# Kernel optimization log

Hardware: AMD Instinct MI355X
Metric: run time of the kernel (lower is better)

Reference implementation:

```python
import jax, jax.numpy as jnp
import numpy as np

HEADS = 8
BLOCK = 32

def setup_inputs() -> dict:
    key = jax.random.key(0)
    ks = jax.random.split(key, 4)
    b, n, d, f = 4, 4096, 1024, 128
    x = jax.random.normal(ks[0], (b, n, d), dtype=jnp.float32)
    w_qkv = jax.random.normal(ks[1], (3 * d, d), dtype=jnp.float32) * (d ** -0.5)
    w_out = jax.random.normal(ks[2], (d, d), dtype=jnp.float32) * (d ** -0.5)
    b_out = jnp.zeros((d,), dtype=jnp.float32)
    proj = jax.random.normal(ks[3], (HEADS, d // HEADS, f), dtype=jnp.float32) * ((d // HEADS) ** -0.5)
    return {"x": x, "w_qkv": w_qkv, "w_out": w_out, "b_out": b_out, "proj": proj}

def reference(x, w_qkv, w_out, b_out, proj):
    b, n, d = x.shape
    h = HEADS
    hd = d // h
    nb = n // BLOCK
    # QKV projection (torch Linear: x @ W.T)
    qkv = x @ w_qkv.T  # (b, n, 3d)
    q, k, v = jnp.split(qkv, 3, axis=-1)
    def to_blocks(t):
        # (b, n, d) -> (b, h, nb, BLOCK, hd)
        return t.reshape(b, n, h, hd).transpose(0, 2, 1, 3).reshape(b, h, nb, BLOCK, hd)
    q, k, v = to_blocks(q), to_blocks(k), to_blocks(v)
    # per-head feature map: elu(x @ proj) + 1
    qp = jax.nn.elu(jnp.einsum('bhcsd,hdf->bhcsf', q, proj)) + 1.0
    kp = jax.nn.elu(jnp.einsum('bhcsd,hdf->bhcsf', k, proj)) + 1.0
    # per-block kv state and normalizer
    kv = jnp.einsum('bhcsf,bhcsd->bhcfd', kp, v)          # (b,h,nb,f,hd)
    num = jnp.einsum('bhcsf,bhcfd->bhcsd', qp, kv)        # (b,h,nb,BLOCK,hd)
    ksum = kp.sum(axis=3)                                 # (b,h,nb,f)
    z = 1.0 / (jnp.einsum('bhcsf,bhcf->bhcs', qp, ksum) + 1e-8)
    out = num * z[..., None]
    # merge blocks and heads: (b,h,nb,BLOCK,hd) -> (b,n,d)
    out = out.reshape(b, h, n, hd).transpose(0, 2, 1, 3).reshape(b, n, d)
    # output projection (dropout inert in eval)
    return out @ w_out.T + b_out
```

## Files before the change

kernel.cpp:

```cpp
#include <hip/hip_runtime.h>
#include <hip/hip_bf16.h>
#include <stdint.h>
#include <stddef.h>

typedef __bf16 bf16_t;
typedef __bf16 bf16x8 __attribute__((ext_vector_type(8)));
typedef __bf16 bf16x4 __attribute__((ext_vector_type(4)));
typedef float  f32x4  __attribute__((ext_vector_type(4)));

static __device__ __forceinline__ f32x4 mfma16x16x32(bf16x8 a, bf16x8 b, f32x4 c) {
  return __builtin_amdgcn_mfma_f32_16x16x32_bf16(a, b, c, 0, 0, 0);
}

static __device__ __forceinline__ void gld_lds16(const void* g, void* l) {
  __builtin_amdgcn_global_load_lds(
      (const __attribute__((address_space(1))) unsigned int*)g,
      (__attribute__((address_space(3))) unsigned int*)l, 16, 0, 0);
}

#define BARW()   __builtin_amdgcn_s_barrier()
#define SCHED0() __builtin_amdgcn_sched_barrier(0)
#define LGKM0()  asm volatile("s_waitcnt lgkmcnt(0)" ::: "memory")
#define LGKMN(n) asm volatile("s_waitcnt lgkmcnt(" #n ")" ::: "memory")
#define VMCNT(n) asm volatile("s_waitcnt vmcnt(" #n ")" ::: "memory")
#define PRIO(p)  __builtin_amdgcn_s_setprio(p)

__global__ __launch_bounds__(256) void prep(const float* __restrict__ wqkv,
                                            const float* __restrict__ proj,
                                            const float* __restrict__ wout,
                                            const float* __restrict__ x,
                                            bf16_t* __restrict__ B1t2,
                                            bf16_t* __restrict__ Wv,
                                            bf16_t* __restrict__ W3t,
                                            bf16_t* __restrict__ xbf) {
  const int b = blockIdx.x;
  const int tid = threadIdx.x;
  if (b >= 1536) {
    for (int i = (b - 1536) * 256 + tid; i < 4194304; i += 262144) {
      float4 v = *(const float4*)(x + (size_t)i * 4);
      bf16x4 o;
      o[0] = (bf16_t)v.x; o[1] = (bf16_t)v.y; o[2] = (bf16_t)v.z; o[3] = (bf16_t)v.w;
      *(bf16x4*)(xbf + (size_t)i * 4) = o;
    }
    return;
  }
  if (b >= 1024) {
    const float* src = (b < 1280) ? wout : (wqkv + (size_t)2048 * 1024);
    bf16_t* dst = (b < 1280) ? W3t : Wv;
    size_t off = ((size_t)((b - 1024) & 255) * 4096) + tid * 16;
#pragma unroll
    for (int it = 0; it < 4; ++it) {
      float4 v = *(const float4*)(src + off + it * 4);
      bf16x4 o;
      o[0] = (bf16_t)v.x; o[1] = (bf16_t)v.y; o[2] = (bf16_t)v.z; o[3] = (bf16_t)v.w;
      *(bf16x4*)(dst + off + it * 4) = o;
    }
    return;
  }
  const int combo = b >> 6;
  const int kt    = (b >> 2) & 15;
  const int fq    = b & 3;
  const int qk    = combo >> 3;
  const int h     = combo & 7;
  const int klocal = tid & 63;
  const int fg     = tid >> 6;
  const int k      = kt * 64 + klocal;

  const float* wbase = wqkv + ((size_t)(qk * 1024 + h * 128)) * 1024 + k;
  const float* pbase = proj + (size_t)h * 16384 + fq * 32 + fg * 8;

  float acc[8];
#pragma unroll
  for (int i = 0; i < 8; ++i) acc[i] = 0.f;

  for (int c = 0; c < 128; ++c) {
    float a = wbase[(size_t)c * 1024];
    const float4* p = (const float4*)(pbase + (size_t)c * 128);
    float4 p0 = p[0], p1 = p[1];
    acc[0] += a * p0.x; acc[1] += a * p0.y; acc[2] += a * p0.z; acc[3] += a * p0.w;
    acc[4] += a * p1.x; acc[5] += a * p1.y; acc[6] += a * p1.z; acc[7] += a * p1.w;
  }
  bf16_t* obase = B1t2 + ((size_t)(h * 256 + qk * 128 + fq * 32 + fg * 8)) * 1024 + k;
#pragma unroll
  for (int i = 0; i < 8; ++i) obase[(size_t)i * 1024] = (bf16_t)acc[i];
}

#define GEMM_MAINLOOP_DECLS()                                                  \
  const int tid  = threadIdx.x;                                                \
  const int lane = tid & 63;                                                   \
  const int wid  = tid >> 6;                                                   \
  const int wm   = wid >> 2;                                                   \
  const int wn   = wid & 3;                                                    \
  const int lr   = lane & 15;                                                  \
  const int g0   = lane >> 4;                                                  \
  int srow[2], sgl[2];                                                         \
  _Pragma("unroll")                                                            \
  for (int l = 0; l < 2; ++l) {                                                \
    int idx = l * 512 + tid;                                                   \
    srow[l] = idx >> 3;                                                        \
    sgl[l]  = (idx & 7) ^ (srow[l] & 7);                                       \
  }

#define STAGE_T(arr, base, half, kt, K_)                                       \
  {                                                                            \
    const bf16_t* s_ = (base) + (size_t)((half) * 128) * (K_) + (kt) * 64;     \
    bf16_t* d_ = &(arr)[half][0];                                              \
    _Pragma("unroll")                                                          \
    for (int l_ = 0; l_ < 2; ++l_)                                             \
      gld_lds16(s_ + (size_t)srow[l_] * (K_) + sgl[l_] * 8,                    \
                d_ + (l_ * 512 + tid) * 8);                                    \
  }

#define RD_A(buf, qm)                                                          \
  _Pragma("unroll")                                                            \
  for (int t_ = 0; t_ < 4; ++t_) {                                             \
    int r_ = (qm) * 64 + t_ * 16 + lr;                                         \
    _Pragma("unroll")                                                          \
    for (int kh_ = 0; kh_ < 2; ++kh_) {                                        \
      int gl_ = (g0 + kh_ * 4) ^ (r_ & 7);                                     \
      a[t_][kh_] = *(const bf16x8*)(&sA[buf][wm][r_ * 64 + gl_ * 8]);          \
    }                                                                          \
  }
#define RD_B(buf, qn, breg)                                                    \
  _Pragma("unroll")                                                            \
  for (int u_ = 0; u_ < 2; ++u_) {                                             \
    int r_ = (wn & 1) * 64 + (qn) * 32 + u_ * 16 + lr;                         \
    _Pragma("unroll")                                                          \
    for (int kh_ = 0; kh_ < 2; ++kh_) {                                        \
      int gl_ = (g0 + kh_ * 4) ^ (r_ & 7);                                     \
      breg[u_][kh_] = *(const bf16x8*)(&sB[buf][wn >> 1][r_ * 64 + gl_ * 8]);  \
    }                                                                          \
  }
#define MMA(qm, qn, breg)                                                      \
  _Pragma("unroll")                                                            \
  for (int mi_ = 0; mi_ < 4; ++mi_)                                            \
    _Pragma("unroll")                                                          \
    for (int nj_ = 0; nj_ < 2; ++nj_)                                          \
      _Pragma("unroll")                                                        \
      for (int kh_ = 0; kh_ < 2; ++kh_)                                        \
        acc[(qm) * 4 + mi_][(qn) * 2 + nj_] =                                  \
            mfma16x16x32(a[mi_][kh_], breg[nj_][kh_],                          \
                         acc[(qm) * 4 + mi_][(qn) * 2 + nj_]);

#define GEMM_MAINLOOP_BODY(Abase, Bbase, K_, NT_)                              \
  f32x4 acc[8][4] = {};                                                        \
  bf16x8 a[4][2], b0[2][2], b1[2][2];                                          \
  STAGE_T(sA[0], Abase, 0, 0, K_); STAGE_T(sA[0], Abase, 1, 0, K_);            \
  STAGE_T(sB[0], Bbase, 0, 0, K_); STAGE_T(sB[0], Bbase, 1, 0, K_);            \
  STAGE_T(sA[1], Abase, 0, 1, K_); STAGE_T(sA[1], Abase, 1, 1, K_);            \
  STAGE_T(sB[1], Bbase, 0, 1, K_); STAGE_T(sB[1], Bbase, 1, 1, K_);            \
  VMCNT(8);                                                                    \
  BARW();                                                                      \
  _Pragma("unroll 2")                                                          \
  for (int j = 0; j < (NT_); ++j) {                                            \
    const int cur = j & 1;                                                     \
    const bool pf = (j + 2) < (NT_);                                           \
    RD_A(cur, 0);                                                              \
    RD_B(cur, 0, b0);                                                          \
    SCHED0(); LGKMN(8); BARW(); LGKM0(); SCHED0();                             \
    PRIO(1); MMA(0, 0, b0); PRIO(0);                                           \
    SCHED0(); BARW();                                                          \
    RD_B(cur, 1, b1);                                                          \
    SCHED0(); BARW(); LGKM0(); SCHED0();                                       \
    PRIO(1); MMA(0, 1, b1); PRIO(0);                                           \
    SCHED0(); BARW();                                                          \
    RD_A(cur, 1);                                                              \
    if (pf) { STAGE_T(sB[cur], Bbase, 0, j + 2, K_); STAGE_T(sB[cur], Bbase, 1, j + 2, K_); } \
    SCHED0(); LGKMN(4); BARW(); LGKM0(); SCHED0();                             \
    PRIO(1); MMA(1, 1, b1); PRIO(0);                                           \
    SCHED0(); BARW();                                                          \
    if (pf) { STAGE_T(sA[cur], Abase, 0, j + 2, K_); STAGE_T(sA[cur], Abase, 1, j + 2, K_); } \
    SCHED0(); BARW();                                                          \
    PRIO(1); MMA(1, 0, b0); PRIO(0);                                           \
    if (pf) { VMCNT(8); } else { VMCNT(0); }                                   \
    SCHED0(); BARW();                                                          \
  }

template <int EPI>
__global__ __launch_bounds__(512, 2) void gemm256(const bf16_t* __restrict__ A,
                                                  const bf16_t* __restrict__ Bt,
                                                  void* __restrict__ Cout,
                                                  const float* __restrict__ bias,
                                                  int N, int K, int NB) {
  __shared__ __align__(16) bf16_t sA[2][2][8192];
  __shared__ __align__(16) bf16_t sB[2][2][8192];
  GEMM_MAINLOOP_DECLS();

  const int nwg = gridDim.x;
  const int cpx = nwg >> 3;
  const int bid = blockIdx.x;
  const int swz = (bid & 7) * cpx + (bid >> 3);
  const int m0 = (swz / NB) * 256;
  const int n0 = (swz % NB) * 256;
  const int NT = K >> 6;

  const bf16_t* Abase = A  + (size_t)m0 * K;
  const bf16_t* Bbase = Bt + (size_t)n0 * K;

  GEMM_MAINLOOP_BODY(Abase, Bbase, K, NT);

#pragma unroll
  for (int i = 0; i < 8; ++i) {
#pragma unroll
    for (int jn = 0; jn < 4; ++jn) {
      const int n = n0 + wn * 64 + jn * 16 + lr;
#pragma unroll
      for (int r = 0; r < 4; ++r) {
        const int m = m0 + wm * 128 + i * 16 + g0 * 4 + r;
        float v = acc[i][jn][r];
        if constexpr (EPI == 2) {
          ((float*)Cout)[(size_t)m * N + n] = v + bias[n];
        } else {
          ((bf16_t*)Cout)[(size_t)m * N + n] = (bf16_t)v;
        }
      }
    }
  }
}

__global__ __launch_bounds__(512, 2) void gemm_fused(const bf16_t* __restrict__ A,
                                                     const bf16_t* __restrict__ Bt,
                                                     const bf16_t* __restrict__ VtG,
                                                     bf16_t* __restrict__ OUT1) {
  __shared__ __align__(16) bf16_t sA[2][2][8192];
  __shared__ __align__(16) bf16_t sB[2][2][8192];
  GEMM_MAINLOOP_DECLS();

  const int nwg = gridDim.x;
  const int cpx = nwg >> 3;
  const int bid = blockIdx.x;
  const int swz = (bid & 7) * cpx + (bid >> 3);
  const int m0 = (swz >> 3) * 256;
  const int h  = swz & 7;
  const int K  = 1024;
  const int NT = 16;

  const bf16_t* Abase = A  + (size_t)m0 * K;
  const bf16_t* Bbase = Bt + (size_t)(h * 256) * K;

  GEMM_MAINLOOP_BODY(Abase, Bbase, K, NT);

  char* sQb = (char*)(&sA[0][0][0]);
  char* sKb = (char*)(&sB[0][0][0]);

  {
    char* dbase = (wn < 2) ? sQb : sKb;
#pragma unroll
    for (int i = 0; i < 8; ++i)
#pragma unroll
      for (int jn = 0; jn < 4; ++jn)
#pragma unroll
        for (int r = 0; r < 4; ++r) {
          int row = wm * 128 + i * 16 + g0 * 4 + r;
          int col = (wn & 1) * 64 + jn * 16 + lr;
          float v = acc[i][jn][r];
          v = v > 0.f ? v + 1.f : __expf(v);
          int gq = col >> 3;
          int g  = (gq & 8) | ((gq ^ row) & 7);
          *(bf16_t*)(dbase + row * 256 + g * 16 + (col & 7) * 2) = (bf16_t)v;
        }
  }
  LGKM0();
  BARW();

  const int cb = wm * 4 + wn;
  const int rb = cb * 32;
  bf16x8 aS[4][2], bS[4][2];
#pragma unroll
  for (int kh = 0; kh < 4; ++kh) {
#pragma unroll
    for (int t = 0; t < 2; ++t) {
      int row = rb + t * 16 + lr;
      int gq = kh * 4 + g0;
      int g  = (gq & 8) | ((gq ^ row) & 7);
      aS[kh][t] = *(const bf16x8*)(sQb + row * 256 + g * 16);
      bS[kh][t] = *(const bf16x8*)(sKb + row * 256 + g * 16);
    }
  }
  SCHED0(); LGKM0(); BARW();

  {
#pragma unroll
    for (int l = 0; l < 8; ++l) {
      int gd = l * 512 + tid;
      int row = gd >> 5, gcol = gd & 31;
      const bf16_t* src = VtG + (size_t)(h * 128 + row) * 16384 + m0 +
                          ((gcol ^ (row & 7)) * 8);
      gld_lds16(src, sKb + gd * 16);
    }
  }
  SCHED0();

  f32x4 sacc[2][2] = {};
#pragma unroll
  for (int kh = 0; kh < 4; ++kh)
#pragma unroll
    for (int mt = 0; mt < 2; ++mt)
#pragma unroll
      for (int nt = 0; nt < 2; ++nt)
        sacc[mt][nt] = mfma16x16x32(aS[kh][mt], bS[kh][nt], sacc[mt][nt]);

  float zin[2][4];
#pragma unroll
  for (int mt = 0; mt < 2; ++mt)
#pragma unroll
    for (int r = 0; r < 4; ++r) {
      float s = sacc[mt][0][r] + sacc[mt][1][r];
      s += __shfl_xor(s, 1); s += __shfl_xor(s, 2);
      s += __shfl_xor(s, 4); s += __shfl_xor(s, 8);
      zin[mt][r] = 1.0f / (s + 1e-8f);
    }

  char* Pl = sQb;
#pragma unroll
  for (int mt = 0; mt < 2; ++mt)
#pragma unroll
    for (int nt = 0; nt < 2; ++nt)
#pragma unroll
      for (int r = 0; r < 4; ++r) {
        int i = mt * 16 + g0 * 4 + r;
        int jj = nt * 16 + lr;
        *(bf16_t*)(Pl + cb * 2560 + i * 80 + jj * 2) =
            (bf16_t)(sacc[mt][nt][r] * zin[mt][r]);
      }
  LGKM0();
  VMCNT(0);
  BARW();

  bf16x8 aP[2];
#pragma unroll
  for (int mt = 0; mt < 2; ++mt)
    aP[mt] = *(const bf16x8*)(Pl + cb * 2560 + (mt * 16 + lr) * 80 + g0 * 16);
#pragma unroll
  for (int dt = 0; dt < 8; ++dt) {
    int row = dt * 16 + lr;
    int gidx = cb * 4 + g0;
    int g = (gidx & 24) | ((gidx ^ row) & 7);
    bf16x8 bV = *(const bf16x8*)(sKb + row * 512 + g * 16);
#pragma unroll
    for (int mt = 0; mt < 2; ++mt) {
      f32x4 z = {};
      f32x4 o = mfma16x16x32(aP[mt], bV, z);
#pragma unroll
      for (int r = 0; r < 4; ++r) {
        int m = m0 + rb + mt * 16 + g0 * 4 + r;
        int d = h * 128 + dt * 16 + lr;
        OUT1[(size_t)m * 1024 + d] = (bf16_t)o[r];
      }
    }
  }
}

extern "C" void kernel_launch(void* const* d_in, const int* in_sizes, int n_in,
                              void* d_out, int out_size, void* d_ws, size_t ws_size,
                              hipStream_t stream) {
  const float* x     = (const float*)d_in[0];
  const float* w_qkv = (const float*)d_in[1];
  const float* w_out = (const float*)d_in[2];
  const float* b_out = (const float*)d_in[3];
  const float* proj  = (const float*)d_in[4];
  float* out = (float*)d_out;

  char* ws = (char*)d_ws;
  bf16_t* xbf  = (bf16_t*)(ws);
  bf16_t* B1t2 = (bf16_t*)(ws + 33554432);
  bf16_t* Wv   = (bf16_t*)(ws + 37748736);
  bf16_t* W3t  = (bf16_t*)(ws + 39845888);
  bf16_t* VtG  = (bf16_t*)(ws + 41943040);
  bf16_t* OUT1 = (bf16_t*)(ws + 75497472);

  (void)in_sizes; (void)n_in; (void)out_size; (void)ws_size;

  prep<<<2560, 256, 0, stream>>>(w_qkv, proj, w_out, x, B1t2, Wv, W3t, xbf);
  gemm256<3><<<256, 512, 0, stream>>>(Wv, xbf, (void*)VtG, nullptr, 16384, 1024, 64);
  gemm_fused<<<512, 512, 0, stream>>>(xbf, B1t2, VtG, OUT1);
  gemm256<2><<<256, 512, 0, stream>>>(OUT1, W3t, (void*)out, b_out, 1024, 1024, 4);
}
```

Baseline: 207.8 us.

## Fuse V projection GEMM into fused attention kernel, dropping separate launch

The separate gemm256 launch that computed V^T for all tokens is removed. Each gemm_fused workgroup now computes its own 256-token by 128-dim V^T tile in a preliminary K loop over the same x tile, and writes it in a pre-swizzled per-block layout that is later loaded back into LDS with contiguous addresses. This removes a kernel launch and the strided VtG gather, but adds a second pass over the x tile per workgroup and puts more serial work on each block, so occupancy and load balance may suffer.

```diff
diff --git a/kernel.cpp b/kernel.cpp
--- a/kernel.cpp
+++ b/kernel.cpp
@@ -176,7 +176,6 @@
     SCHED0(); BARW();                                                          \
   }
 
-template <int EPI>
 __global__ __launch_bounds__(512, 2) void gemm256(const bf16_t* __restrict__ A,
                                                   const bf16_t* __restrict__ Bt,
                                                   void* __restrict__ Cout,
@@ -207,12 +206,7 @@
 #pragma unroll
       for (int r = 0; r < 4; ++r) {
         const int m = m0 + wm * 128 + i * 16 + g0 * 4 + r;
-        float v = acc[i][jn][r];
-        if constexpr (EPI == 2) {
-          ((float*)Cout)[(size_t)m * N + n] = v + bias[n];
-        } else {
-          ((bf16_t*)Cout)[(size_t)m * N + n] = (bf16_t)v;
-        }
+        ((float*)Cout)[(size_t)m * N + n] = acc[i][jn][r] + bias[n];
       }
     }
   }
@@ -220,7 +214,8 @@
 
 __global__ __launch_bounds__(512, 2) void gemm_fused(const bf16_t* __restrict__ A,
                                                      const bf16_t* __restrict__ Bt,
-                                                     const bf16_t* __restrict__ VtG,
+                                                     const bf16_t* __restrict__ Wv,
+                                                     bf16_t* __restrict__ VtG,
                                                      bf16_t* __restrict__ OUT1) {
   __shared__ __align__(16) bf16_t sA[2][2][8192];
   __shared__ __align__(16) bf16_t sB[2][2][8192];
@@ -237,6 +232,84 @@
 
   const bf16_t* Abase = A  + (size_t)m0 * K;
   const bf16_t* Bbase = Bt + (size_t)(h * 256) * K;
+  bf16_t* VtGblk = VtG + (size_t)swz * 32768;
+
+  {
+    const bf16_t* Wbase = Wv + (size_t)(h * 128) * 1024;
+    f32x4 accv[4][4] = {};
+    bf16x8 av[4][2], bv[4][2];
+    const int wmv = wid >> 1;
+    const int wnv = wid & 1;
+    const int ah  = wmv >> 1;
+    const int ar0 = (wmv & 1) * 64;
+
+    STAGE_T(sA[0], Abase, 0, 0, K); STAGE_T(sA[0], Abase, 1, 0, K);
+    STAGE_T(sB[0], Wbase, 0, 0, K);
+    STAGE_T(sA[1], Abase, 0, 1, K); STAGE_T(sA[1], Abase, 1, 1, K);
+    STAGE_T(sB[1], Wbase, 0, 1, K);
+    VMCNT(6);
+    BARW();
+#pragma unroll 2
+    for (int j = 0; j < NT; ++j) {
+      const int cur = j & 1;
+      const bool pf = (j + 2) < NT;
+#pragma unroll
+      for (int mi = 0; mi < 4; ++mi) {
+        int r_ = ar0 + mi * 16 + lr;
+#pragma unroll
+        for (int kh = 0; kh < 2; ++kh) {
+          int gl = (g0 + kh * 4) ^ (r_ & 7);
+          av[mi][kh] = *(const bf16x8*)(&sA[cur][ah][r_ * 64 + gl * 8]);
+        }
+      }
+#pragma unroll
+      for (int di = 0; di < 4; ++di) {
+        int r_ = wnv * 64 + di * 16 + lr;
+#pragma unroll
+        for (int kh = 0; kh < 2; ++kh) {
+          int gl = (g0 + kh * 4) ^ (r_ & 7);
+          bv[di][kh] = *(const bf16x8*)(&sB[cur][0][r_ * 64 + gl * 8]);
+        }
+      }
+      SCHED0(); LGKMN(8); BARW(); LGKM0(); SCHED0();
+      PRIO(1);
+#pragma unroll
+      for (int mi = 0; mi < 4; ++mi)
+#pragma unroll
+        for (int di = 0; di < 2; ++di)
+#pragma unroll
+          for (int kh = 0; kh < 2; ++kh)
+            accv[mi][di] = mfma16x16x32(av[mi][kh], bv[di][kh], accv[mi][di]);
+      PRIO(0);
+      if (pf) { STAGE_T(sB[cur], Wbase, 0, j + 2, K); }
+      SCHED0(); BARW();
+      PRIO(1);
+#pragma unroll
+      for (int mi = 0; mi < 4; ++mi)
+#pragma unroll
+        for (int di = 2; di < 4; ++di)
+#pragma unroll
+          for (int kh = 0; kh < 2; ++kh)
+            accv[mi][di] = mfma16x16x32(av[mi][kh], bv[di][kh], accv[mi][di]);
+      PRIO(0);
+      if (pf) { STAGE_T(sA[cur], Abase, 0, j + 2, K); STAGE_T(sA[cur], Abase, 1, j + 2, K); }
+      if (pf) { VMCNT(6); } else { VMCNT(0); }
+      SCHED0(); BARW();
+    }
+#pragma unroll
+    for (int mi = 0; mi < 4; ++mi)
+#pragma unroll
+      for (int di = 0; di < 4; ++di) {
+        int d  = wnv * 64 + di * 16 + lr;
+        int mb = wmv * 64 + mi * 16 + g0 * 4;
+        int c  = mb >> 3;
+        int g  = (c & 24) | ((c ^ d) & 7);
+        bf16x4 pk;
+#pragma unroll
+        for (int r = 0; r < 4; ++r) pk[r] = (bf16_t)accv[mi][di][r];
+        *(bf16x4*)((char*)VtGblk + d * 512 + g * 16 + (mb & 7) * 2) = pk;
+      }
+  }
 
   GEMM_MAINLOOP_BODY(Abase, Bbase, K, NT);
 
@@ -283,10 +356,7 @@
 #pragma unroll
     for (int l = 0; l < 8; ++l) {
       int gd = l * 512 + tid;
-      int row = gd >> 5, gcol = gd & 31;
-      const bf16_t* src = VtG + (size_t)(h * 128 + row) * 16384 + m0 +
-                          ((gcol ^ (row & 7)) * 8);
-      gld_lds16(src, sKb + gd * 16);
+      gld_lds16(VtGblk + (size_t)gd * 8, sKb + gd * 16);
     }
   }
   SCHED0();
@@ -372,7 +442,6 @@
   (void)in_sizes; (void)n_in; (void)out_size; (void)ws_size;
 
   prep<<<2560, 256, 0, stream>>>(w_qkv, proj, w_out, x, B1t2, Wv, W3t, xbf);
-  gemm256<3><<<256, 512, 0, stream>>>(Wv, xbf, (void*)VtG, nullptr, 16384, 1024, 64);
-  gemm_fused<<<512, 512, 0, stream>>>(xbf, B1t2, VtG, OUT1);
-  gemm256<2><<<256, 512, 0, stream>>>(OUT1, W3t, (void*)out, b_out, 1024, 1024, 4);
-}
+  gemm_fused<<<512, 512, 0, stream>>>(xbf, B1t2, Wv, VtG, OUT1);
+  gemm256<<<256, 512, 0, stream>>>(OUT1, W3t, (void*)out, b_out, 1024, 1024, 4);
+}
```

Result: faster. 200.0 us (median of 2 runs) (-3.7%).
